# Optimization experiments

Measured on AMD Instinct MI355X. Metric: run time of the kernel, lower is better.

Reference implementation:

```python
import jax, jax.numpy as jnp
import numpy as np

NUM_SEQS = 8
SEQ_LEN = 2048
HIDDEN = 768
NUM_HEADS = 12
HEAD_DIM = 64
EPS = 1e-12


def setup_inputs() -> dict:
    key = jax.random.key(0)
    ks = jax.random.split(key, 12)
    total = NUM_SEQS * SEQ_LEN
    hidden_states = jax.random.normal(ks[0], (total, HIDDEN), dtype=jnp.float32)
    cu_seq_lens = jnp.arange(NUM_SEQS + 1, dtype=jnp.int32) * SEQ_LEN
    s = 0.02
    inp = {
        "hidden_states": hidden_states,
        "cu_seq_lens": cu_seq_lens,
        "max_seq_len": SEQ_LEN,
        "norm_w": jnp.ones((HIDDEN,), jnp.float32),
        "norm_b": jnp.zeros((HIDDEN,), jnp.float32),
        "Wq": jax.random.normal(ks[1], (HIDDEN, HIDDEN), jnp.float32) * s,
        "bq": jnp.zeros((HIDDEN,), jnp.float32),
        "Wk": jax.random.normal(ks[2], (HIDDEN, HIDDEN), jnp.float32) * s,
        "bk": jnp.zeros((HIDDEN,), jnp.float32),
        "Wv": jax.random.normal(ks[3], (HIDDEN, HIDDEN), jnp.float32) * s,
        "bv": jnp.zeros((HIDDEN,), jnp.float32),
        "Wo": jax.random.normal(ks[4], (HIDDEN, HIDDEN), jnp.float32) * s,
        "bo": jnp.zeros((HIDDEN,), jnp.float32),
    }
    return inp


def _layer_norm(x, w, b):
    mu = jnp.mean(x, axis=-1, keepdims=True)
    var = jnp.mean(jnp.square(x - mu), axis=-1, keepdims=True)
    return (x - mu) * jax.lax.rsqrt(var + EPS) * w + b


def _rope(x, positions, interleaved=False):
    # x: [t, h, d]; positions: [t]
    d = x.shape[-1]
    inv_freq = 1.0 / (10000.0 ** (jnp.arange(0, d, 2, dtype=jnp.float32) / d))  # [d/2]
    theta = positions.astype(jnp.float32)[:, None] * inv_freq[None, :]  # [t, d/2]
    cos = jnp.cos(theta)[:, None, :]  # [t, 1, d/2]
    sin = jnp.sin(theta)[:, None, :]
    x1, x2 = x[..., : d // 2], x[..., d // 2 :]
    return jnp.concatenate([x1 * cos - x2 * sin, x2 * cos + x1 * sin], axis=-1)


def _attention(q, k, v):
    # q,k,v: [b, s, h, d] (equal-length sequences, no padding)
    scale = 1.0 / jnp.sqrt(jnp.asarray(q.shape[-1], q.dtype))
    scores = jnp.einsum("bqhd,bkhd->bhqk", q, k) * scale
    probs = jax.nn.softmax(scores, axis=-1)
    return jnp.einsum("bhqk,bkhd->bqhd", probs, v)


def reference(hidden_states, cu_seq_lens, max_seq_len, norm_w, norm_b,
              Wq, bq, Wk, bk, Wv, bv, Wo, bo):
    t = hidden_states.shape[0]
    # pre_norm, layer_idx=1 -> LayerNorm
    x = _layer_norm(hidden_states, norm_w, norm_b)
    value = x @ Wv + bv
    query = x @ Wq + bq
    key = x @ Wk + bk

    def split(z):
        return z.reshape(t, NUM_HEADS, HEAD_DIM)

    q, k, v = split(query), split(key), split(value)

    # positions within each sequence (equal-length packing)
    positions = jnp.tile(jnp.arange(SEQ_LEN, dtype=jnp.int32), NUM_SEQS)
    q = _rope(q, positions)
    k = _rope(k, positions)

    # reshape packed -> [b, s, h, d]; sequences are equal-length here
    qb = q.reshape(NUM_SEQS, SEQ_LEN, NUM_HEADS, HEAD_DIM)
    kb = k.reshape(NUM_SEQS, SEQ_LEN, NUM_HEADS, HEAD_DIM)
    vb = v.reshape(NUM_SEQS, SEQ_LEN, NUM_HEADS, HEAD_DIM)
    attn = _attention(qb, kb, vb).reshape(t, HIDDEN)

    attn = attn @ Wo + bo
    # residual add (dropout prob = 0)
    out = attn + x
    return out
```

## Files before the change

kernel.cpp:

```cpp
#include <hip/hip_runtime.h>

typedef __bf16 bf16x8 __attribute__((ext_vector_type(8)));
typedef float  f32x4  __attribute__((ext_vector_type(4)));
typedef float  f32x16 __attribute__((ext_vector_type(16)));
typedef unsigned u32x2 __attribute__((ext_vector_type(2)));

#define MFMA16(a,b,c) __builtin_amdgcn_mfma_f32_16x16x32_bf16((a),(b),(c),0,0,0)
#define MFMA32(a,b,c) __builtin_amdgcn_mfma_f32_32x32x16_bf16((a),(b),(c),0,0,0)

constexpr int  HID  = 768;
constexpr long T    = 16384;
constexpr long SZ   = T * HID;
constexpr int  SEQ  = 2048;
constexpr int  NH   = 12;
constexpr int  HD   = 64;
constexpr int  WELE = HID * HID;

constexpr float QSCALE = 0.125f * 1.4426950408889634f;
constexpr float L10K32 = 13.287712379549449f / 32.0f;

__device__ __forceinline__ unsigned pkbf(float a, float b) {
    union { __bf16 h[2]; unsigned u; } x;
    x.h[0] = (__bf16)a; x.h[1] = (__bf16)b; return x.u;
}

__device__ __forceinline__ void gld16(const __bf16* g, __bf16* l) {
    __builtin_amdgcn_global_load_lds(
        (const __attribute__((address_space(1))) unsigned int*)g,
        (__attribute__((address_space(3))) unsigned int*)l, 16, 0, 0);
}

#define WAITVN(N) asm volatile("s_waitcnt vmcnt(" #N ")" ::: "memory")
#define BARR()    asm volatile("s_barrier" ::: "memory")

__global__ __launch_bounds__(256)
void wconv_kernel(const float* __restrict__ W0, __bf16* __restrict__ T0,
                  const float* __restrict__ W1, __bf16* __restrict__ T1,
                  const float* __restrict__ W2, __bf16* __restrict__ T2,
                  const float* __restrict__ W3, __bf16* __restrict__ T3) {
    const float* W; __bf16* Wt;
    switch (blockIdx.z) {
        case 0: W = W0; Wt = T0; break;
        case 1: W = W1; Wt = T1; break;
        case 2: W = W2; Wt = T2; break;
        default: W = W3; Wt = T3; break;
    }
    __shared__ float tile[64][65];
    int n0 = blockIdx.x * 64, k0 = blockIdx.y * 64;
    int c = threadIdx.x & 63, rr = threadIdx.x >> 6;
#pragma unroll
    for (int i = 0; i < 16; i++) {
        int r = i * 4 + rr;
        tile[r][c] = W[(long)(k0 + r) * HID + n0 + c];
    }
    __syncthreads();
#pragma unroll
    for (int i = 0; i < 16; i++) {
        int r = i * 4 + rr;
        Wt[(long)(n0 + r) * HID + k0 + c] = (__bf16)tile[c][r];
    }
}

__global__ __launch_bounds__(256)
void ln_kernel(const float* __restrict__ hs, const float* __restrict__ w,
               const float* __restrict__ b, __bf16* __restrict__ xbf) {
    int row = blockIdx.x, tid = threadIdx.x;
    const float* hr = hs + (long)row * HID;
    float v0 = hr[tid], v1 = hr[tid + 256], v2 = hr[tid + 512];
    float s  = v0 + v1 + v2;
    float s2 = v0 * v0 + v1 * v1 + v2 * v2;
#pragma unroll
    for (int off = 1; off < 64; off <<= 1) {
        s  += __shfl_xor(s, off);
        s2 += __shfl_xor(s2, off);
    }
    __shared__ float red[8];
    int wave = tid >> 6;
    if ((tid & 63) == 0) { red[wave] = s; red[4 + wave] = s2; }
    __syncthreads();
    s  = red[0] + red[1] + red[2] + red[3];
    s2 = red[4] + red[5] + red[6] + red[7];
    float mu   = s * (1.0f / HID);
    float var  = s2 * (1.0f / HID) - mu * mu;
    float rstd = rsqrtf(var + 1e-12f);
    long base = (long)row * HID;
    xbf[base + tid]       = (__bf16)((v0 - mu) * rstd * w[tid]       + b[tid]);
    xbf[base + tid + 256] = (__bf16)((v1 - mu) * rstd * w[tid + 256] + b[tid + 256]);
    xbf[base + tid + 512] = (__bf16)((v2 - mu) * rstd * w[tid + 512] + b[tid + 512]);
}

constexpr int SEGSZ = 528;
constexpr int BUFSZ = 16 * SEGSZ;

template <int MODE>
__global__ __launch_bounds__(256)
void gemm_lds(const __bf16* __restrict__ A, const __bf16* __restrict__ Bt,
              const float* __restrict__ bias, __bf16* __restrict__ outb,
              const __bf16* __restrict__ resid, float* __restrict__ outf,
              float scale) {
    int tid = threadIdx.x, wave = tid >> 6, lane = tid & 63;
    int lr = lane & 15, quad = lane >> 4;
    int wm = wave >> 1, wn = wave & 1;
    long m0 = (long)blockIdx.x * 128;
    int  n0 = blockIdx.y * 128;

    __shared__ __align__(16) __bf16 As[2][BUFSZ];
    __shared__ __align__(16) __bf16 Bs[2][BUFSZ];

    const f32x4 vzero = {0.f, 0.f, 0.f, 0.f};
    f32x4 acc[4][4];
#pragma unroll
    for (int ms = 0; ms < 4; ms++)
#pragma unroll
        for (int ns = 0; ns < 4; ns++) acc[ms][ns] = vzero;

    const __bf16* ga = A  + (long)(m0 + wave * 32 + (lane >> 3)) * HID + (lane & 7) * 8;
    const __bf16* gb = Bt + (long)(n0 + wave * 32 + (lane >> 3)) * HID + (lane & 7) * 8;

    int fbase = (lr >> 3) * SEGSZ + (lr & 7) * 64 + quad * 8;

#define GSTAGE(b, k0)                                                           \
    {                                                                           \
        _Pragma("unroll")                                                       \
        for (int j = 0; j < 4; j++) {                                           \
            gld16(ga + (long)j * 8 * HID + (k0), As[b] + wave * 4 * SEGSZ + j * SEGSZ); \
            gld16(gb + (long)j * 8 * HID + (k0), Bs[b] + wave * 4 * SEGSZ + j * SEGSZ); \
        }                                                                       \
    }

#define GCOMP(b)                                                                \
    {                                                                           \
        _Pragma("unroll")                                                       \
        for (int kk = 0; kk < 64; kk += 32) {                                   \
            bf16x8 af[4], bfr[4];                                               \
            _Pragma("unroll")                                                   \
            for (int ms = 0; ms < 4; ms++)                                      \
                af[ms] = *(const bf16x8*)&As[b][fbase + (wm * 8 + ms * 2) * SEGSZ + kk]; \
            _Pragma("unroll")                                                   \
            for (int ns = 0; ns < 4; ns++)                                      \
                bfr[ns] = *(const bf16x8*)&Bs[b][fbase + (wn * 8 + ns * 2) * SEGSZ + kk]; \
            _Pragma("unroll")                                                   \
            for (int ms = 0; ms < 4; ms++)                                      \
                _Pragma("unroll")                                               \
                for (int ns = 0; ns < 4; ns++)                                  \
                    acc[ms][ns] = MFMA16(af[ms], bfr[ns], acc[ms][ns]);         \
        }                                                                       \
    }

    GSTAGE(0, 0)
#pragma unroll 1
    for (int u = 0; u < 5; u++) {
        int k0 = u * 128;
        GSTAGE(1, k0 + 64)  WAITVN(8); BARR(); GCOMP(0) BARR();
        GSTAGE(0, k0 + 128) WAITVN(8); BARR(); GCOMP(1) BARR();
    }
    GSTAGE(1, 11 * 64) WAITVN(8); BARR(); GCOMP(0) BARR();
    WAITVN(0); BARR(); GCOMP(1)

#undef GSTAGE
#undef GCOMP

    if (MODE == 1) {
#pragma unroll
        for (int ms = 0; ms < 4; ms++)
#pragma unroll
        for (int r = 0; r < 4; r++) {
            int d = (int)(m0 + wm * 64 + ms * 16 + quad * 4 + r);
            float bv = bias[d];
            int hh = d >> 6, dd = d & 63;
#pragma unroll
            for (int ns = 0; ns < 4; ns++) {
                int posg = n0 + wn * 64 + ns * 16 + lr;
                int sq = posg >> 11, pos = posg & (SEQ - 1);
                outb[((long)((sq * NH + hh) * HD + dd) << 11) + pos] =
                    (__bf16)(acc[ms][ns][r] + bv);
            }
        }
    } else {
#pragma unroll
        for (int ns = 0; ns < 4; ns++) {
            int col = n0 + wn * 64 + ns * 16 + lr;
            float bv = bias[col];
#pragma unroll
            for (int ms = 0; ms < 4; ms++)
#pragma unroll
            for (int r = 0; r < 4; r++) {
                long row = m0 + wm * 64 + ms * 16 + quad * 4 + r;
                outf[row * HID + col] = acc[ms][ns][r] + bv + (float)resid[row * HID + col];
            }
        }
    }
}

__global__ __launch_bounds__(256, 2)
void gemm_qk(const __bf16* __restrict__ A, const __bf16* __restrict__ Btq,
             const __bf16* __restrict__ Btk,
             const float* __restrict__ biasq, const float* __restrict__ biask,
             __bf16* __restrict__ outq, __bf16* __restrict__ outk) {
    int tid = threadIdx.x, wave = tid >> 6, lane = tid & 63;
    int lr = lane & 15, quad = lane >> 4;
    int wm = wave >> 1, wn = wave & 1;
    long m0 = (long)blockIdx.x * 128;
    int  n0 = blockIdx.y * 128;

    __shared__ __align__(16) __bf16 As[2][BUFSZ];
    __shared__ __align__(16) __bf16 Bqs[BUFSZ];
    __shared__ __align__(16) __bf16 Bks[BUFSZ];

    const f32x4 vzero = {0.f, 0.f, 0.f, 0.f};
    f32x4 accq[4][4], acck[4][4];
#pragma unroll
    for (int ms = 0; ms < 4; ms++)
#pragma unroll
        for (int ns = 0; ns < 4; ns++) { accq[ms][ns] = vzero; acck[ms][ns] = vzero; }

    const __bf16* ga = A   + (long)(m0 + wave * 32 + (lane >> 3)) * HID + (lane & 7) * 8;
    const __bf16* gq = Btq + (long)(n0 + wave * 32 + (lane >> 3)) * HID + (lane & 7) * 8;
    const __bf16* gk = Btk + (long)(n0 + wave * 32 + (lane >> 3)) * HID + (lane & 7) * 8;

    int fbase = (lr >> 3) * SEGSZ + (lr & 7) * 64 + quad * 8;

#define QSTAGE_A(b, k0)                                                         \
    {                                                                           \
        _Pragma("unroll")                                                       \
        for (int j = 0; j < 4; j++)                                             \
            gld16(ga + (long)j * 8 * HID + (k0), As[b] + wave * 4 * SEGSZ + j * SEGSZ); \
    }
#define QSTAGE_B(k0)                                                            \
    {                                                                           \
        _Pragma("unroll")                                                       \
        for (int j = 0; j < 4; j++) {                                           \
            gld16(gq + (long)j * 8 * HID + (k0), Bqs + wave * 4 * SEGSZ + j * SEGSZ); \
            gld16(gk + (long)j * 8 * HID + (k0), Bks + wave * 4 * SEGSZ + j * SEGSZ); \
        }                                                                       \
    }
#define QCOMP(b)                                                                \
    {                                                                           \
        _Pragma("unroll")                                                       \
        for (int kk = 0; kk < 64; kk += 32) {                                   \
            bf16x8 af[4], bqf[4], bkf[4];                                       \
            _Pragma("unroll")                                                   \
            for (int ms = 0; ms < 4; ms++)                                      \
                af[ms] = *(const bf16x8*)&As[b][fbase + (wm * 8 + ms * 2) * SEGSZ + kk]; \
            _Pragma("unroll")                                                   \
            for (int ns = 0; ns < 4; ns++) {                                    \
                bqf[ns] = *(const bf16x8*)&Bqs[fbase + (wn * 8 + ns * 2) * SEGSZ + kk]; \
                bkf[ns] = *(const bf16x8*)&Bks[fbase + (wn * 8 + ns * 2) * SEGSZ + kk]; \
            }                                                                   \
            _Pragma("unroll")                                                   \
            for (int ms = 0; ms < 4; ms++)                                      \
                _Pragma("unroll")                                               \
                for (int ns = 0; ns < 4; ns++) {                                \
                    accq[ms][ns] = MFMA16(af[ms], bqf[ns], accq[ms][ns]);       \
                    acck[ms][ns] = MFMA16(af[ms], bkf[ns], acck[ms][ns]);       \
                }                                                               \
        }                                                                       \
    }

    QSTAGE_A(0, 0) QSTAGE_B(0) QSTAGE_A(1, 64)
    WAITVN(4); BARR();

#pragma unroll 1
    for (int u = 0; u < 5; u++) {
        int k0 = u * 128;
        QCOMP(0) BARR();
        QSTAGE_B(k0 + 64)  QSTAGE_A(0, k0 + 128) WAITVN(4); BARR();
        QCOMP(1) BARR();
        QSTAGE_B(k0 + 128) QSTAGE_A(1, k0 + 192) WAITVN(4); BARR();
    }
    QCOMP(0) BARR();
    QSTAGE_B(11 * 64) WAITVN(0); BARR();
    QCOMP(1)

#undef QSTAGE_A
#undef QSTAGE_B
#undef QCOMP

    int hb = n0 + wn * 64;
    float f1 = __builtin_amdgcn_exp2f(-(float)lr * L10K32);
    float f2 = __builtin_amdgcn_exp2f(-(float)(lr + 16) * L10K32);
    {
        float b0 = biasq[hb + lr],      b1 = biasq[hb + 16 + lr];
        float b2 = biasq[hb + 32 + lr], b3 = biasq[hb + 48 + lr];
#pragma unroll
        for (int ms = 0; ms < 4; ms++)
#pragma unroll
        for (int r = 0; r < 4; r++) {
            long row = m0 + wm * 64 + ms * 16 + quad * 4 + r;
            int pos = (int)(row & (SEQ - 1));
            float s1, c1, s2, c2;
            __sincosf((float)pos * f1, &s1, &c1);
            __sincosf((float)pos * f2, &s2, &c2);
            float v0 = accq[ms][0][r] + b0, v1 = accq[ms][1][r] + b1;
            float v2 = accq[ms][2][r] + b2, v3 = accq[ms][3][r] + b3;
            __bf16* ob = outq + row * HID + hb;
            ob[lr]      = (__bf16)((v0 * c1 - v2 * s1) * QSCALE);
            ob[16 + lr] = (__bf16)((v1 * c2 - v3 * s2) * QSCALE);
            ob[32 + lr] = (__bf16)((v2 * c1 + v0 * s1) * QSCALE);
            ob[48 + lr] = (__bf16)((v3 * c2 + v1 * s2) * QSCALE);
        }
    }
    {
        float b0 = biask[hb + lr],      b1 = biask[hb + 16 + lr];
        float b2 = biask[hb + 32 + lr], b3 = biask[hb + 48 + lr];
#pragma unroll
        for (int ms = 0; ms < 4; ms++)
#pragma unroll
        for (int r = 0; r < 4; r++) {
            long row = m0 + wm * 64 + ms * 16 + quad * 4 + r;
            int pos = (int)(row & (SEQ - 1));
            float s1, c1, s2, c2;
            __sincosf((float)pos * f1, &s1, &c1);
            __sincosf((float)pos * f2, &s2, &c2);
            float v0 = acck[ms][0][r] + b0, v1 = acck[ms][1][r] + b1;
            float v2 = acck[ms][2][r] + b2, v3 = acck[ms][3][r] + b3;
            __bf16* ob = outk + row * HID + hb;
            ob[lr]      = (__bf16)(v0 * c1 - v2 * s1);
            ob[16 + lr] = (__bf16)(v1 * c2 - v3 * s2);
            ob[32 + lr] = (__bf16)(v2 * c1 + v0 * s1);
            ob[48 + lr] = (__bf16)(v3 * c2 + v1 * s2);
        }
    }
}

__global__ __launch_bounds__(512)
void attn_kernel(const __bf16* __restrict__ q, const __bf16* __restrict__ k,
                 const __bf16* __restrict__ vt, __bf16* __restrict__ att) {
    int tid = threadIdx.x, wave = tid >> 6, lane = tid & 63;
    int c = lane & 31, hi = lane >> 5;
    int bb = blockIdx.x;
    int s  = bb & 7;
    int ii = bb >> 3;
    int h  = ii >> 3;
    int qt = ii & 7;
    long q0 = (long)s * SEQ + qt * 256 + wave * 32;

    __shared__ __align__(16) __bf16 KV[6 * 4096];

    bf16x8 qf[4];
    {
        const __bf16* qrow = q + (q0 + c) * HID + h * HD + hi * 8;
#pragma unroll
        for (int kk = 0; kk < 4; kk++)
            qf[kk] = *(const bf16x8*)(qrow + kk * 16);
    }

    f32x16 o[2] = {};
    float ls = 0.f;

    const __bf16* kg = k  + (long)s * SEQ * HID + h * HD;
    const __bf16* vg = vt + (long)(s * NH + h) * HD * SEQ;

    int srow = lane >> 3;
    int sgch = (lane & 7) ^ srow;

    const __bf16* pb4[4];
#pragma unroll
    for (int kk = 0; kk < 4; kk++)
        pb4[kk] = KV + c * 64 + ((((kk << 1) + hi) ^ (c & 7)) << 3);

#define STAGE(bufi, kv)                                                         \
    {                                                                           \
        gld16(kg + (long)((kv) + wave * 8 + srow) * HID + sgch * 8,             \
              KV + (bufi) * 4096 + wave * 512);                                 \
        gld16(vg + (long)(wave * 8 + srow) * SEQ + (kv) + sgch * 8,             \
              KV + 12288 + (bufi) * 4096 + wave * 512);                         \
    }

#define ATTN_BODY(BUF)                                                          \
    {                                                                           \
        f32x16 st0 = {}, st1 = {};                                              \
        __builtin_amdgcn_s_setprio(1);                                          \
        _Pragma("unroll")                                                       \
        for (int kk = 0; kk < 4; kk++) {                                        \
            bf16x8 kf0 = *(const bf16x8*)(pb4[kk] + (BUF) * 4096);              \
            st0 = MFMA32(kf0, qf[kk], st0);                                     \
            bf16x8 kf1 = *(const bf16x8*)(pb4[kk] + (BUF) * 4096 + 2048);       \
            st1 = MFMA32(kf1, qf[kk], st1);                                     \
        }                                                                       \
        __builtin_amdgcn_s_setprio(0);                                          \
        bf16x8 pb[4];                                                           \
        _Pragma("unroll")                                                       \
        for (int kh = 0; kh < 2; kh++) {                                        \
            unsigned pk[8];                                                     \
            _Pragma("unroll")                                                   \
            for (int i = 0; i < 8; i++) {                                       \
                float e0 = __builtin_amdgcn_exp2f(kh ? st1[2 * i] : st0[2 * i]);        \
                float e1 = __builtin_amdgcn_exp2f(kh ? st1[2 * i + 1] : st0[2 * i + 1]);\
                ls += e0 + e1;                                                  \
                pk[i] = pkbf(e0, e1);                                           \
            }                                                                   \
            _Pragma("unroll")                                                   \
            for (int b = 0; b < 2; b++) {                                       \
                u32x2 r02 = __builtin_amdgcn_permlane32_swap(                   \
                    pk[4 * b + 0], pk[4 * b + 2], false, false);                \
                u32x2 r13 = __builtin_amdgcn_permlane32_swap(                   \
                    pk[4 * b + 1], pk[4 * b + 3], false, false);                \
                union { unsigned u[4]; bf16x8 v; } pu;                          \
                pu.u[0] = r02[0]; pu.u[1] = r13[0];                             \
                pu.u[2] = r02[1]; pu.u[3] = r13[1];                             \
                pb[2 * kh + b] = pu.v;                                          \
            }                                                                   \
        }                                                                       \
        __builtin_amdgcn_s_setprio(1);                                          \
        _Pragma("unroll")                                                       \
        for (int kk = 0; kk < 4; kk++) {                                        \
            bf16x8 vf0 = *(const bf16x8*)(pb4[kk] + 12288 + (BUF) * 4096);      \
            o[0] = MFMA32(vf0, pb[kk], o[0]);                                   \
            bf16x8 vf1 = *(const bf16x8*)(pb4[kk] + 12288 + (BUF) * 4096 + 2048); \
            o[1] = MFMA32(vf1, pb[kk], o[1]);                                   \
        }                                                                       \
        __builtin_amdgcn_s_setprio(0);                                          \
    }

    STAGE(0, 0)
    STAGE(1, 64)

#pragma unroll 1
    for (int u = 0; u < 10; u++) {
        int kv = u * 3 * 64;
        WAITVN(2); BARR();
        STAGE(2, kv + 2 * 64)
        ATTN_BODY(0)
        WAITVN(2); BARR();
        STAGE(0, kv + 3 * 64)
        ATTN_BODY(1)
        WAITVN(2); BARR();
        STAGE(1, kv + 4 * 64)
        ATTN_BODY(2)
    }
    WAITVN(2); BARR();
    ATTN_BODY(0)
    WAITVN(0); BARR();
    ATTN_BODY(1)

#undef STAGE
#undef ATTN_BODY

    ls += __shfl_xor(ls, 32);
    float inv = 1.0f / ls;
    __bf16* ob = att + (q0 + c) * HID + h * HD;
#pragma unroll
    for (int dh = 0; dh < 2; dh++)
#pragma unroll
        for (int a = 0; a < 4; a++) {
            unsigned lo  = pkbf(o[dh][4 * a] * inv,     o[dh][4 * a + 1] * inv);
            unsigned hi2 = pkbf(o[dh][4 * a + 2] * inv, o[dh][4 * a + 3] * inv);
            int d = dh * 32 + a * 8 + hi * 4;
            *(unsigned long long*)&ob[d] =
                ((unsigned long long)hi2 << 32) | lo;
        }
}

extern "C" void kernel_launch(void* const* d_in, const int* in_sizes, int n_in,
                              void* d_out, int out_size, void* d_ws, size_t ws_size,
                              hipStream_t stream) {
    const float* hs    = (const float*)d_in[0];
    const float* normw = (const float*)d_in[3];
    const float* normb = (const float*)d_in[4];
    const float* Wq = (const float*)d_in[5];
    const float* bq = (const float*)d_in[6];
    const float* Wk = (const float*)d_in[7];
    const float* bk = (const float*)d_in[8];
    const float* Wv = (const float*)d_in[9];
    const float* bv = (const float*)d_in[10];
    const float* Wo = (const float*)d_in[11];
    const float* bo = (const float*)d_in[12];

    __bf16* base = (__bf16*)d_ws;
    __bf16* x   = base;
    __bf16* qb  = base + SZ;
    __bf16* kb  = base + 2 * SZ;
    __bf16* vtb = base + 3 * SZ;
    __bf16* att = base + 4 * SZ;
    __bf16* wqt = base + 5 * SZ;
    __bf16* wkt = wqt + WELE;
    __bf16* wvt = wkt + WELE;
    __bf16* wot = wvt + WELE;

    wconv_kernel<<<dim3(12, 12, 4), 256, 0, stream>>>(Wq, wqt, Wk, wkt, Wv, wvt, Wo, wot);

    ln_kernel<<<(int)T, 256, 0, stream>>>(hs, normw, normb, x);

    gemm_qk<<<dim3(T / 128, HID / 128), 256, 0, stream>>>(x, wqt, wkt, bq, bk, qb, kb);
    gemm_lds<1><<<dim3(HID / 128, T / 128), 256, 0, stream>>>(wvt, x, bv, vtb, nullptr, nullptr, 1.0f);

    attn_kernel<<<dim3(NH * 8 * 8), 512, 0, stream>>>(qb, kb, vtb, att);

    gemm_lds<2><<<dim3(T / 128, HID / 128), 256, 0, stream>>>(att, wot, bo, nullptr, x, (float*)d_out, 1.0f);
}
```

Baseline: 380.7 us.

## Precompute RoPE table and restructure GEMM staging with single-buffered weight tile

```diff
diff --git a/kernel.cpp b/kernel.cpp
--- a/kernel.cpp
+++ b/kernel.cpp
@@ -37,7 +37,22 @@
 void wconv_kernel(const float* __restrict__ W0, __bf16* __restrict__ T0,
                   const float* __restrict__ W1, __bf16* __restrict__ T1,
                   const float* __restrict__ W2, __bf16* __restrict__ T2,
-                  const float* __restrict__ W3, __bf16* __restrict__ T3) {
+                  const float* __restrict__ W3, __bf16* __restrict__ T3,
+                  float* __restrict__ rope) {
+    if (blockIdx.z == 4) {
+        int gid = (blockIdx.y * 12 + blockIdx.x) * 256 + threadIdx.x;
+        if (gid < SEQ * 16) {
+            int pos = gid >> 4, lr = gid & 15;
+            float f1 = __builtin_amdgcn_exp2f(-(float)lr * L10K32);
+            float f2 = __builtin_amdgcn_exp2f(-(float)(lr + 16) * L10K32);
+            float s1, c1, s2, c2;
+            __sincosf((float)pos * f1, &s1, &c1);
+            __sincosf((float)pos * f2, &s2, &c2);
+            f32x4 v = {c1, s1, c2, s2};
+            *(f32x4*)&rope[(long)gid * 4] = v;
+        }
+        return;
+    }
     const float* W; __bf16* Wt;
     switch (blockIdx.z) {
         case 0: W = W0; Wt = T0; break;
@@ -104,8 +119,8 @@
     long m0 = (long)blockIdx.x * 128;
     int  n0 = blockIdx.y * 128;
 
-    __shared__ __align__(16) __bf16 As[2][BUFSZ];
-    __shared__ __align__(16) __bf16 Bs[2][BUFSZ];
+    __shared__ __align__(16) __bf16 Ss[2][BUFSZ];
+    __shared__ __align__(16) __bf16 Ws[BUFSZ];
 
     const f32x4 vzero = {0.f, 0.f, 0.f, 0.f};
     f32x4 acc[4][4];
@@ -116,29 +131,36 @@
 
     const __bf16* ga = A  + (long)(m0 + wave * 32 + (lane >> 3)) * HID + (lane & 7) * 8;
     const __bf16* gb = Bt + (long)(n0 + wave * 32 + (lane >> 3)) * HID + (lane & 7) * 8;
+    const __bf16* gs = (MODE == 2) ? ga : gb;
+    const __bf16* gw = (MODE == 2) ? gb : ga;
 
     int fbase = (lr >> 3) * SEGSZ + (lr & 7) * 64 + quad * 8;
 
-#define GSTAGE(b, k0)                                                           \
-    {                                                                           \
-        _Pragma("unroll")                                                       \
-        for (int j = 0; j < 4; j++) {                                           \
-            gld16(ga + (long)j * 8 * HID + (k0), As[b] + wave * 4 * SEGSZ + j * SEGSZ); \
-            gld16(gb + (long)j * 8 * HID + (k0), Bs[b] + wave * 4 * SEGSZ + j * SEGSZ); \
-        }                                                                       \
-    }
-
+#define SSTAGE(b, k0)                                                           \
+    {                                                                           \
+        _Pragma("unroll")                                                       \
+        for (int j = 0; j < 4; j++)                                             \
+            gld16(gs + (long)j * 8 * HID + (k0), Ss[b] + wave * 4 * SEGSZ + j * SEGSZ); \
+    }
+#define WSTAGE(k0)                                                              \
+    {                                                                           \
+        _Pragma("unroll")                                                       \
+        for (int j = 0; j < 4; j++)                                             \
+            gld16(gw + (long)j * 8 * HID + (k0), Ws + wave * 4 * SEGSZ + j * SEGSZ); \
+    }
 #define GCOMP(b)                                                                \
     {                                                                           \
+        const __bf16* Ab = (MODE == 2) ? &Ss[b][0] : &Ws[0];                    \
+        const __bf16* Bb = (MODE == 2) ? &Ws[0] : &Ss[b][0];                    \
         _Pragma("unroll")                                                       \
         for (int kk = 0; kk < 64; kk += 32) {                                   \
             bf16x8 af[4], bfr[4];                                               \
             _Pragma("unroll")                                                   \
             for (int ms = 0; ms < 4; ms++)                                      \
-                af[ms] = *(const bf16x8*)&As[b][fbase + (wm * 8 + ms * 2) * SEGSZ + kk]; \
+                af[ms] = *(const bf16x8*)&Ab[fbase + (wm * 8 + ms * 2) * SEGSZ + kk]; \
             _Pragma("unroll")                                                   \
             for (int ns = 0; ns < 4; ns++)                                      \
-                bfr[ns] = *(const bf16x8*)&Bs[b][fbase + (wn * 8 + ns * 2) * SEGSZ + kk]; \
+                bfr[ns] = *(const bf16x8*)&Bb[fbase + (wn * 8 + ns * 2) * SEGSZ + kk]; \
             _Pragma("unroll")                                                   \
             for (int ms = 0; ms < 4; ms++)                                      \
                 _Pragma("unroll")                                               \
@@ -147,17 +169,23 @@
         }                                                                       \
     }
 
-    GSTAGE(0, 0)
+    SSTAGE(0, 0) WSTAGE(0) SSTAGE(1, 64)
+    WAITVN(4); BARR();
+
 #pragma unroll 1
     for (int u = 0; u < 5; u++) {
         int k0 = u * 128;
-        GSTAGE(1, k0 + 64)  WAITVN(8); BARR(); GCOMP(0) BARR();
-        GSTAGE(0, k0 + 128) WAITVN(8); BARR(); GCOMP(1) BARR();
-    }
-    GSTAGE(1, 11 * 64) WAITVN(8); BARR(); GCOMP(0) BARR();
-    WAITVN(0); BARR(); GCOMP(1)
-
-#undef GSTAGE
+        GCOMP(0) BARR();
+        WSTAGE(k0 + 64)  SSTAGE(0, k0 + 128) WAITVN(4); BARR();
+        GCOMP(1) BARR();
+        WSTAGE(k0 + 128) SSTAGE(1, k0 + 192) WAITVN(4); BARR();
+    }
+    GCOMP(0) BARR();
+    WSTAGE(11 * 64) WAITVN(0); BARR();
+    GCOMP(1)
+
+#undef SSTAGE
+#undef WSTAGE
 #undef GCOMP
 
     if (MODE == 1) {
@@ -196,7 +224,8 @@
 void gemm_qk(const __bf16* __restrict__ A, const __bf16* __restrict__ Btq,
              const __bf16* __restrict__ Btk,
              const float* __restrict__ biasq, const float* __restrict__ biask,
-             __bf16* __restrict__ outq, __bf16* __restrict__ outk) {
+             __bf16* __restrict__ outq, __bf16* __restrict__ outk,
+             const float* __restrict__ rope) {
     int tid = threadIdx.x, wave = tid >> 6, lane = tid & 63;
     int lr = lane & 15, quad = lane >> 4;
     int wm = wave >> 1, wn = wave & 1;
@@ -277,43 +306,30 @@
 #undef QCOMP
 
     int hb = n0 + wn * 64;
-    float f1 = __builtin_amdgcn_exp2f(-(float)lr * L10K32);
-    float f2 = __builtin_amdgcn_exp2f(-(float)(lr + 16) * L10K32);
-    {
-        float b0 = biasq[hb + lr],      b1 = biasq[hb + 16 + lr];
-        float b2 = biasq[hb + 32 + lr], b3 = biasq[hb + 48 + lr];
-#pragma unroll
-        for (int ms = 0; ms < 4; ms++)
-#pragma unroll
-        for (int r = 0; r < 4; r++) {
-            long row = m0 + wm * 64 + ms * 16 + quad * 4 + r;
-            int pos = (int)(row & (SEQ - 1));
-            float s1, c1, s2, c2;
-            __sincosf((float)pos * f1, &s1, &c1);
-            __sincosf((float)pos * f2, &s2, &c2);
-            float v0 = accq[ms][0][r] + b0, v1 = accq[ms][1][r] + b1;
-            float v2 = accq[ms][2][r] + b2, v3 = accq[ms][3][r] + b3;
+    float q0b = biasq[hb + lr],      q1b = biasq[hb + 16 + lr];
+    float q2b = biasq[hb + 32 + lr], q3b = biasq[hb + 48 + lr];
+    float k0b = biask[hb + lr],      k1b = biask[hb + 16 + lr];
+    float k2b = biask[hb + 32 + lr], k3b = biask[hb + 48 + lr];
+#pragma unroll
+    for (int ms = 0; ms < 4; ms++)
+#pragma unroll
+    for (int r = 0; r < 4; r++) {
+        long row = m0 + wm * 64 + ms * 16 + quad * 4 + r;
+        int pos = (int)(row & (SEQ - 1));
+        f32x4 tb = *(const f32x4*)&rope[((long)pos * 16 + lr) * 4];
+        float c1 = tb[0], s1 = tb[1], c2 = tb[2], s2 = tb[3];
+        {
+            float v0 = accq[ms][0][r] + q0b, v1 = accq[ms][1][r] + q1b;
+            float v2 = accq[ms][2][r] + q2b, v3 = accq[ms][3][r] + q3b;
             __bf16* ob = outq + row * HID + hb;
             ob[lr]      = (__bf16)((v0 * c1 - v2 * s1) * QSCALE);
             ob[16 + lr] = (__bf16)((v1 * c2 - v3 * s2) * QSCALE);
             ob[32 + lr] = (__bf16)((v2 * c1 + v0 * s1) * QSCALE);
             ob[48 + lr] = (__bf16)((v3 * c2 + v1 * s2) * QSCALE);
         }
-    }
-    {
-        float b0 = biask[hb + lr],      b1 = biask[hb + 16 + lr];
-        float b2 = biask[hb + 32 + lr], b3 = biask[hb + 48 + lr];
-#pragma unroll
-        for (int ms = 0; ms < 4; ms++)
-#pragma unroll
-        for (int r = 0; r < 4; r++) {
-            long row = m0 + wm * 64 + ms * 16 + quad * 4 + r;
-            int pos = (int)(row & (SEQ - 1));
-            float s1, c1, s2, c2;
-            __sincosf((float)pos * f1, &s1, &c1);
-            __sincosf((float)pos * f2, &s2, &c2);
-            float v0 = acck[ms][0][r] + b0, v1 = acck[ms][1][r] + b1;
-            float v2 = acck[ms][2][r] + b2, v3 = acck[ms][3][r] + b3;
+        {
+            float v0 = acck[ms][0][r] + k0b, v1 = acck[ms][1][r] + k1b;
+            float v2 = acck[ms][2][r] + k2b, v3 = acck[ms][3][r] + k3b;
             __bf16* ob = outk + row * HID + hb;
             ob[lr]      = (__bf16)(v0 * c1 - v2 * s1);
             ob[16 + lr] = (__bf16)(v1 * c2 - v3 * s2);
@@ -477,12 +493,13 @@
     __bf16* wkt = wqt + WELE;
     __bf16* wvt = wkt + WELE;
     __bf16* wot = wvt + WELE;
-
-    wconv_kernel<<<dim3(12, 12, 4), 256, 0, stream>>>(Wq, wqt, Wk, wkt, Wv, wvt, Wo, wot);
+    float*  rope = (float*)(wot + WELE);
+
+    wconv_kernel<<<dim3(12, 12, 5), 256, 0, stream>>>(Wq, wqt, Wk, wkt, Wv, wvt, Wo, wot, rope);
 
     ln_kernel<<<(int)T, 256, 0, stream>>>(hs, normw, normb, x);
 
-    gemm_qk<<<dim3(T / 128, HID / 128), 256, 0, stream>>>(x, wqt, wkt, bq, bk, qb, kb);
+    gemm_qk<<<dim3(T / 128, HID / 128), 256, 0, stream>>>(x, wqt, wkt, bq, bk, qb, kb, rope);
     gemm_lds<1><<<dim3(HID / 128, T / 128), 256, 0, stream>>>(wvt, x, bv, vtb, nullptr, nullptr, 1.0f);
 
     attn_kernel<<<dim3(NH * 8 * 8), 512, 0, stream>>>(qb, kb, vtb, att);
```

Result: no change. 379.8 us (-0.3%).
